# Kernel tuning notes

Hardware: AMD Instinct MI355X
Metric: run time of the kernel (lower is better)

The kernel has to match this reference:

```python
import jax, jax.numpy as jnp
import numpy as np

EPS_LN = 1e-6
EPS_NORM = 1e-12
MAX_SCALE_MUL = float(np.log(100.0))
H = 16  # num_heads


def _ln(x):
    # affine-free LayerNorm over last dim (torch uses biased variance)
    mu = jnp.mean(x, axis=-1, keepdims=True)
    var = jnp.mean((x - mu) ** 2, axis=-1, keepdims=True)
    return (x - mu) / jnp.sqrt(var + EPS_LN)


def _l2norm(x):
    n = jnp.sqrt(jnp.sum(x * x, axis=-1, keepdims=True))
    return x / jnp.maximum(n, EPS_NORM)


def setup_inputs() -> dict:
    key = jax.random.key(0)
    ks = jax.random.split(key, 12)
    B, L, C = 4, 1024, 1024
    Ccond, Dff = 1024, 4096
    s = lambda fan: 1.0 / np.sqrt(fan)
    return {
        "x": jax.random.normal(ks[0], (B, L, C), jnp.float32),
        "cond": jax.random.normal(ks[1], (B, Ccond), jnp.float32),
        "mat_qkv_w": jax.random.normal(ks[2], (3 * C, C), jnp.float32) * s(C),
        "q_bias": jnp.zeros((C,), jnp.float32),
        "v_bias": jnp.zeros((C,), jnp.float32),
        "scale_mul": jnp.full((1, H, 1, 1), np.log(4.0), jnp.float32),
        "proj_w": jax.random.normal(ks[3], (C, C), jnp.float32) * s(C),
        "proj_b": jnp.zeros((C,), jnp.float32),
        "ada_w": jax.random.normal(ks[4], (6 * C, Ccond), jnp.float32) * s(Ccond),
        "ada_b": jnp.zeros((6 * C,), jnp.float32),
        "fc1_w": jax.random.normal(ks[5], (Dff, C), jnp.float32) * s(C),
        "fc1_b": jnp.zeros((Dff,), jnp.float32),
        "fc2_w": jax.random.normal(ks[6], (C, Dff), jnp.float32) * s(Dff),
        "fc2_b": jnp.zeros((C,), jnp.float32),
    }


def reference(x, cond, mat_qkv_w, q_bias, v_bias, scale_mul, proj_w, proj_b,
              ada_w, ada_b, fc1_w, fc1_b, fc2_w, fc2_b):
    B, L, C = x.shape
    hd = C // H

    # AdaLN modulation params: SiLU -> Linear -> [B,1,6,C]
    ada = jax.nn.silu(cond) @ ada_w.T + ada_b
    ada = ada.reshape(B, 1, 6, C)
    gamma1, gamma2, scale1, scale2, shift1, shift2 = [ada[:, :, i] for i in range(6)]

    # --- attention branch ---
    x1 = _ln(x) * (scale1 + 1.0) + shift1
    qkv_bias = jnp.concatenate([q_bias, jnp.zeros_like(q_bias), v_bias])
    qkv = (x1 @ mat_qkv_w.T + qkv_bias).reshape(B, L, 3, H, hd)
    q, k, v = [jnp.transpose(qkv[:, :, i], (0, 2, 1, 3)) for i in range(3)]  # [B,H,L,hd]

    sm = jnp.exp(jnp.minimum(scale_mul, MAX_SCALE_MUL))  # [1,H,1,1]
    q = _l2norm(q) * sm
    k = _l2norm(k)

    scores = jnp.einsum('bhqd,bhkd->bhqk', q, k)  # scale = 1.0 under l2 norm
    probs = jax.nn.softmax(scores, axis=-1)
    o = jnp.einsum('bhqk,bhkd->bhqd', probs, v)
    o = jnp.transpose(o, (0, 2, 1, 3)).reshape(B, L, C)
    attn_out = o @ proj_w.T + proj_b
    x = x + attn_out * gamma1

    # --- FFN branch ---
    x2 = _ln(x) * (scale2 + 1.0) + shift2
    h = jax.nn.gelu(x2 @ fc1_w.T + fc1_b, approximate=False)
    ffn_out = h @ fc2_w.T + fc2_b
    x = x + ffn_out * gamma2
    return x
```

## Files before the change

kernel.cpp:

```cpp
#include <hip/hip_runtime.h>

typedef __bf16 bf16x8_t __attribute__((ext_vector_type(8)));
typedef bf16x8_t bf16x8 __attribute__((may_alias));
typedef float f32x4 __attribute__((ext_vector_type(4)));
typedef unsigned short u16x4 __attribute__((ext_vector_type(4)));
typedef unsigned short u16x8 __attribute__((ext_vector_type(8)));

#define DEV __device__ __forceinline__

DEV float b2f(unsigned short u) {
  union { unsigned int i; float f; } x; x.i = ((unsigned int)u) << 16; return x.f;
}
DEV unsigned short f2b(float f) {
  union { float f; unsigned int i; } x; x.f = f;
  return (unsigned short)((x.i + 0x7fffu + ((x.i >> 16) & 1u)) >> 16);
}

#define AS1(p) ((__attribute__((address_space(1))) void*)(p))
#define AS3(p) ((__attribute__((address_space(3))) void*)(p))

__global__ __launch_bounds__(256) void k_ada(const float* __restrict__ cond,
                                             const float* __restrict__ w,
                                             const float* __restrict__ bias,
                                             float* __restrict__ out) {
  __shared__ float sc[4096];
  int tt = threadIdx.x;
#pragma unroll
  for (int i = 0; i < 16; ++i) {
    float v = cond[tt + i * 256];
    sc[tt + i * 256] = v / (1.f + __expf(-v));
  }
  __syncthreads();
  int j = blockIdx.x * 4 + (tt >> 6);
  int lane = tt & 63;
  const float* wr = w + (size_t)j * 1024;
  float s0 = 0.f, s1 = 0.f, s2 = 0.f, s3 = 0.f;
#pragma unroll
  for (int u = 0; u < 4; ++u) {
    int k = u * 256 + lane * 4;
    float4 a = *(const float4*)(wr + k);
    float4 c0 = *(const float4*)(sc + k);
    float4 c1 = *(const float4*)(sc + 1024 + k);
    float4 c2 = *(const float4*)(sc + 2048 + k);
    float4 c3 = *(const float4*)(sc + 3072 + k);
    s0 += a.x * c0.x + a.y * c0.y + a.z * c0.z + a.w * c0.w;
    s1 += a.x * c1.x + a.y * c1.y + a.z * c1.z + a.w * c1.w;
    s2 += a.x * c2.x + a.y * c2.y + a.z * c2.z + a.w * c2.w;
    s3 += a.x * c3.x + a.y * c3.y + a.z * c3.z + a.w * c3.w;
  }
#pragma unroll
  for (int o = 1; o < 64; o <<= 1) {
    s0 += __shfl_xor(s0, o); s1 += __shfl_xor(s1, o);
    s2 += __shfl_xor(s2, o); s3 += __shfl_xor(s3, o);
  }
  if (lane == 0) {
    float bb = bias[j];
    out[j] = s0 + bb;
    out[6144 + j] = s1 + bb;
    out[12288 + j] = s2 + bb;
    out[18432 + j] = s3 + bb;
  }
}

__global__ __launch_bounds__(256) void k_castall(const float* __restrict__ q,
                                                 const float* __restrict__ p,
                                                 const float* __restrict__ f1,
                                                 const float* __restrict__ f2,
                                                 unsigned short* __restrict__ wq,
                                                 unsigned short* __restrict__ wp,
                                                 unsigned short* __restrict__ wf1,
                                                 unsigned short* __restrict__ wf2) {
  int i = blockIdx.x * 256 + threadIdx.x;
  for (int v = i; v < 3145728; v += 524288) {
    const float* s; unsigned short* d; int off;
    if (v < 786432) { s = q; d = wq; off = v; }
    else if (v < 1048576) { s = p; d = wp; off = v - 786432; }
    else if (v < 2097152) { s = f1; d = wf1; off = v - 1048576; }
    else { s = f2; d = wf2; off = v - 2097152; }
    float4 x = ((const float4*)s)[off];
    u16x4 o;
    o[0] = f2b(x.x); o[1] = f2b(x.y); o[2] = f2b(x.z); o[3] = f2b(x.w);
    *(u16x4*)(d + (size_t)off * 4) = o;
  }
}

__global__ __launch_bounds__(256) void k_ln_mod(const float* __restrict__ src,
                                                const float* __restrict__ ada,
                                                unsigned short* __restrict__ dst,
                                                int sidx, int hidx) {
  int row = blockIdx.x;
  int b = row >> 10;
  int t = threadIdx.x, lane = t & 63, wv = t >> 6;
  float4 v = *(const float4*)(src + (size_t)row * 1024 + t * 4);
  float s = v.x + v.y + v.z + v.w;
  float s2 = v.x * v.x + v.y * v.y + v.z * v.z + v.w * v.w;
#pragma unroll
  for (int o = 1; o < 64; o <<= 1) { s += __shfl_xor(s, o); s2 += __shfl_xor(s2, o); }
  __shared__ float red[8];
  if (lane == 0) { red[wv] = s; red[4 + wv] = s2; }
  __syncthreads();
  float ts = red[0] + red[1] + red[2] + red[3];
  float ts2 = red[4] + red[5] + red[6] + red[7];
  float mu = ts * (1.f / 1024.f);
  float var = ts2 * (1.f / 1024.f) - mu * mu;
  float rstd = rsqrtf(var + 1e-6f);
  const float* ar = ada + (size_t)b * 6144;
  float4 sc = *(const float4*)(ar + sidx * 1024 + t * 4);
  float4 sh = *(const float4*)(ar + hidx * 1024 + t * 4);
  u16x4 o;
  o[0] = f2b((v.x - mu) * rstd * (sc.x + 1.f) + sh.x);
  o[1] = f2b((v.y - mu) * rstd * (sc.y + 1.f) + sh.y);
  o[2] = f2b((v.z - mu) * rstd * (sc.z + 1.f) + sh.z);
  o[3] = f2b((v.w - mu) * rstd * (sc.w + 1.f) + sh.w);
  *(u16x4*)(dst + (size_t)row * 1024 + t * 4) = o;
}

template <int EPI, int SPLIT>
__global__ __launch_bounds__(512, 1) void k_gemm256(const unsigned short* __restrict__ A,
                                                    const unsigned short* __restrict__ W,
                                                    int N, int lda, int ldb, int nt,
                                                    const float* __restrict__ bias,
                                                    const float* __restrict__ qb,
                                                    const float* __restrict__ vb,
                                                    unsigned short* __restrict__ o0,
                                                    unsigned short* __restrict__ o1,
                                                    unsigned short* __restrict__ o2,
                                                    unsigned short* __restrict__ o3) {
  __shared__ unsigned short LDS[65536];
  const int tid = threadIdx.x;
  const int wv = tid >> 6, lane = tid & 63;
  const int fr = lane & 15, fg = lane >> 4;
  const int wm = wv >> 2, wn = wv & 3;

  const int cpx = gridDim.x >> 3;
  int wid = ((int)blockIdx.x & 7) * cpx + ((int)blockIdx.x >> 3);
  int sp = 0;
  if (SPLIT > 1) { sp = wid & (SPLIT - 1); wid >>= 2; }
  const int nx = N >> 8;
  const int m0 = (wid / nx) * 256, n0 = (wid % nx) * 256;
  const int kbase = sp * (nt << 6);
  unsigned short* outp = (SPLIT > 1) ? (sp == 0 ? o0 : sp == 1 ? o1 : sp == 2 ? o2 : o3) : o0;

  const int sRow = lane >> 2;
  const int sCh = (lane & 3) ^ ((lane >> 3) & 3);
  const unsigned short* aG = A + (size_t)(m0 + wv * 16 + sRow) * lda + kbase + sCh * 8;
  const unsigned short* bG = W + (size_t)(n0 + wv * 16 + sRow) * ldb + kbase + sCh * 8;

#define STQ4(qi_)                                                                              \
  {                                                                                            \
    const int wr_ = ((qi_)&3) * 16384;                                                         \
    const int ko_ = (qi_)*32;                                                                  \
    __builtin_amdgcn_global_load_lds(AS1(aG + ko_), AS3(LDS + wr_ + wv * 512), 16, 0, 0);      \
    __builtin_amdgcn_global_load_lds(AS1(aG + (size_t)128 * lda + ko_),                        \
                                     AS3(LDS + wr_ + 4096 + wv * 512), 16, 0, 0);              \
    __builtin_amdgcn_global_load_lds(AS1(bG + ko_), AS3(LDS + wr_ + 8192 + wv * 512), 16, 0, 0);\
    __builtin_amdgcn_global_load_lds(AS1(bG + (size_t)128 * ldb + ko_),                        \
                                     AS3(LDS + wr_ + 12288 + wv * 512), 16, 0, 0);             \
  }

  const int rswz = (fr >> 1) & 3;
  const int aOff = (wm * 128 + fr) * 32 + ((fg ^ rswz) << 3);
  const int bOff = 8192 + (wn * 64 + fr) * 32 + ((fg ^ rswz) << 3);

  f32x4 zz = {0.f, 0.f, 0.f, 0.f};
  f32x4 acc[8][4];
#pragma unroll
  for (int i = 0; i < 8; ++i)
#pragma unroll
    for (int j = 0; j < 4; ++j) acc[i][j] = zz;

  STQ4(0); STQ4(1); STQ4(2); STQ4(3);
  asm volatile("s_waitcnt vmcnt(8)" ::: "memory");
  __builtin_amdgcn_s_barrier();

#define LDSV(off) (*(const bf16x8*)(LDS + (off)))

  const int nIv = nt;
  for (int iv = 0; iv < nIv; ++iv) {
    if (iv >= 1) {
      const int t2 = 2 * iv + 2;
      if (t2 < 2 * nt) { STQ4(t2); STQ4(t2 + 1); }
    }
#pragma unroll
    for (int half = 0; half < 2; ++half) {
      const int rb = ((2 * iv + half) & 3) * 16384;
      bf16x8 bf0 = LDSV(rb + bOff);
      bf16x8 bf1 = LDSV(rb + bOff + 512);
      bf16x8 bf2 = LDSV(rb + bOff + 1024);
      bf16x8 bf3 = LDSV(rb + bOff + 1536);
      bf16x8 af[8];
#pragma unroll
      for (int mi = 0; mi < 8; ++mi) af[mi] = LDSV(rb + aOff + mi * 512);
#pragma unroll
      for (int mi = 0; mi < 8; ++mi) {
        acc[mi][0] = __builtin_amdgcn_mfma_f32_16x16x32_bf16(af[mi], bf0, acc[mi][0], 0, 0, 0);
        acc[mi][1] = __builtin_amdgcn_mfma_f32_16x16x32_bf16(af[mi], bf1, acc[mi][1], 0, 0, 0);
        acc[mi][2] = __builtin_amdgcn_mfma_f32_16x16x32_bf16(af[mi], bf2, acc[mi][2], 0, 0, 0);
        acc[mi][3] = __builtin_amdgcn_mfma_f32_16x16x32_bf16(af[mi], bf3, acc[mi][3], 0, 0, 0);
      }
    }
    if (iv < nIv - 1) {
      asm volatile("s_waitcnt vmcnt(0)" ::: "memory");
      __builtin_amdgcn_s_barrier();
    }
  }

#pragma unroll
  for (int mi = 0; mi < 8; ++mi) {
#pragma unroll
    for (int ni = 0; ni < 4; ++ni) {
#pragma unroll
      for (int r = 0; r < 4; ++r) {
        int m = m0 + wm * 128 + mi * 16 + fg * 4 + r;
        int n = n0 + wn * 64 + ni * 16 + fr;
        float v = acc[mi][ni][r];
        if constexpr (EPI == 0) {
          float bb = (n < 1024) ? qb[n] : ((n < 2048) ? 0.f : vb[n - 2048]);
          outp[(size_t)m * N + n] = f2b(v + bb);
        } else if constexpr (EPI == 2) {
          float z = v + bias[n];
          float u = z * (0.7978845608f + 0.0356774081f * z * z);
          float e = __expf(2.f * u);
          float th = 1.f - 2.f / (e + 1.f);
          outp[(size_t)m * N + n] = f2b(0.5f * z * (1.f + th));
        } else {
          outp[(size_t)m * N + n] = f2b(v);
        }
      }
    }
  }
#undef STQ4
#undef LDSV
}

__global__ __launch_bounds__(256) void k_fc2red(const unsigned short* __restrict__ P0,
                                                const unsigned short* __restrict__ P1,
                                                const unsigned short* __restrict__ P2,
                                                const unsigned short* __restrict__ P3,
                                                const float* __restrict__ xmid,
                                                const float* __restrict__ bias,
                                                const float* __restrict__ ada,
                                                float* __restrict__ out) {
  size_t idx = ((size_t)blockIdx.x * 256 + threadIdx.x) * 8;
  int n = (int)(idx & 1023);
  int b = (int)(idx >> 20);
  u16x8 v0 = *(const u16x8*)(P0 + idx);
  u16x8 v1 = *(const u16x8*)(P1 + idx);
  u16x8 v2 = *(const u16x8*)(P2 + idx);
  u16x8 v3 = *(const u16x8*)(P3 + idx);
  const float* gp = ada + (size_t)b * 6144 + 1024 + n;
  const float* bp = bias + n;
  const float* xp = xmid + idx;
  float* op = out + idx;
#pragma unroll
  for (int i = 0; i < 8; ++i) {
    float sum = b2f(v0[i]) + b2f(v1[i]) + b2f(v2[i]) + b2f(v3[i]);
    op[i] = xp[i] + (sum + bp[i]) * gp[i];
  }
}

__global__ __launch_bounds__(512) void k_gemm8(const unsigned short* __restrict__ A,
                                               const unsigned short* __restrict__ W,
                                               int M, int N, int K, int Khalf,
                                               const float* __restrict__ bias,
                                               const float* __restrict__ resid,
                                               const float* __restrict__ ada,
                                               float* __restrict__ outp) {
  __shared__ unsigned short SM[49152];
  const int t = threadIdx.x, lane = t & 63, wv = t >> 6;
  const int grp = wv >> 2, w4 = wv & 3;
  const int wr = w4 >> 1, wc = w4 & 1;
  const int cpx = gridDim.x >> 3;
  const int orig = blockIdx.x;
  const int wid = (orig & 7) * cpx + (orig >> 3);
  const int nx = N >> 7;
  const int m0 = (wid / nx) * 128, n0 = (wid % nx) * 128;

  f32x4 zz = {0.f, 0.f, 0.f, 0.f};
  f32x4 acc[4][4];
#pragma unroll
  for (int i = 0; i < 4; ++i)
#pragma unroll
    for (int j = 0; j < 4; ++j) acc[i][j] = zz;

  const int srow = lane >> 2, scol = (lane & 3) * 8;
  const int kbase = grp * Khalf;
  const unsigned short* aSrc0 = A + (size_t)(m0 + w4 * 16 + srow) * K + kbase + scol;
  const unsigned short* aSrc1 = aSrc0 + (size_t)64 * K;
  const unsigned short* bSrc0 = W + (size_t)(n0 + w4 * 16 + srow) * K + kbase + scol;
  const unsigned short* bSrc1 = bSrc0 + (size_t)64 * K;
  unsigned short* grpA = SM + grp * 24576;

  const int fr = lane & 15, fk = (lane >> 4) * 8;

#define STG8(buf_, k0_)                                                                            \
  {                                                                                                \
    __builtin_amdgcn_global_load_lds(AS1(aSrc0 + (k0_)), AS3(grpA + (buf_)*8192 + w4 * 512), 16, 0, 0); \
    __builtin_amdgcn_global_load_lds(AS1(aSrc1 + (k0_)), AS3(grpA + (buf_)*8192 + 2048 + w4 * 512), 16, 0, 0); \
    __builtin_amdgcn_global_load_lds(AS1(bSrc0 + (k0_)), AS3(grpA + (buf_)*8192 + 4096 + w4 * 512), 16, 0, 0); \
    __builtin_amdgcn_global_load_lds(AS1(bSrc1 + (k0_)), AS3(grpA + (buf_)*8192 + 6144 + w4 * 512), 16, 0, 0); \
  }

  const int nsteps = Khalf >> 5;
  STG8(0, 0);
  STG8(1, 32);
  asm volatile("s_waitcnt vmcnt(4)" ::: "memory");
  __builtin_amdgcn_s_barrier();

  for (int i = 0; i < nsteps; ++i) {
    const int buf = i % 3;
    if (i + 2 < nsteps) STG8((i + 2) % 3, (i + 2) * 32);
    const unsigned short* aRd = grpA + buf * 8192 + (wr * 64 + fr) * 32 + fk;
    const unsigned short* bRd = grpA + buf * 8192 + 4096 + (wc * 64 + fr) * 32 + fk;
    bf16x8 af[4], bfv[4];
#pragma unroll
    for (int q = 0; q < 4; ++q) af[q] = *(const bf16x8*)(aRd + q * 512);
#pragma unroll
    for (int q = 0; q < 4; ++q) bfv[q] = *(const bf16x8*)(bRd + q * 512);
#pragma unroll
    for (int mi = 0; mi < 4; ++mi)
#pragma unroll
      for (int ni = 0; ni < 4; ++ni)
        acc[mi][ni] = __builtin_amdgcn_mfma_f32_16x16x32_bf16(af[mi], bfv[ni], acc[mi][ni], 0, 0, 0);
    if (i < nsteps - 1) {
      if (i + 2 < nsteps) {
        asm volatile("s_waitcnt vmcnt(4)" ::: "memory");
      } else {
        asm volatile("s_waitcnt vmcnt(0)" ::: "memory");
      }
      __builtin_amdgcn_s_barrier();
    }
  }
  __syncthreads();

  float* xch = (float*)SM;
#pragma unroll
  for (int c = 0; c < 16; ++c) {
    if (grp == 1)
      *(f32x4*)&xch[c * 1024 + (w4 * 64 + lane) * 4] = acc[c >> 2][c & 3];
  }
  __syncthreads();
  if (grp == 1) return;
#pragma unroll
  for (int c = 0; c < 16; ++c) {
    f32x4 p = *(const f32x4*)&xch[c * 1024 + (w4 * 64 + lane) * 4];
    acc[c >> 2][c & 3] += p;
  }

  const int fg = lane >> 4;
#pragma unroll
  for (int mi = 0; mi < 4; ++mi) {
#pragma unroll
    for (int ni = 0; ni < 4; ++ni) {
#pragma unroll
      for (int r = 0; r < 4; ++r) {
        int m = m0 + wr * 64 + mi * 16 + fg * 4 + r;
        int n = n0 + wc * 64 + ni * 16 + fr;
        float v = acc[mi][ni][r];
        float g = ada[(size_t)(m >> 10) * 6144 + n];
        outp[(size_t)m * N + n] = resid[(size_t)m * N + n] + (v + bias[n]) * g;
      }
    }
  }
#undef STG8
}

__global__ __launch_bounds__(256) void k_qknorm(const unsigned short* __restrict__ qkv,
                                                const float* __restrict__ smul,
                                                unsigned short* __restrict__ Qn,
                                                unsigned short* __restrict__ Kn) {
  int row = blockIdx.x;
  int b = row >> 10, l = row & 1023;
  int t = threadIdx.x;
  int h = t >> 4, sl = t & 15;
  const unsigned short* base = qkv + (size_t)row * 3072 + h * 64 + sl * 4;
  size_t off = ((size_t)(b * 16 + h) * 1024 + l) * 64 + sl * 4;
  {
    u16x4 qv = *(const u16x4*)base;
    float q0 = b2f(qv[0]), q1 = b2f(qv[1]), q2 = b2f(qv[2]), q3 = b2f(qv[3]);
    float ss = q0 * q0 + q1 * q1 + q2 * q2 + q3 * q3;
#pragma unroll
    for (int o = 1; o < 16; o <<= 1) ss += __shfl_xor(ss, o);
    float sm = __expf(fminf(smul[h], 4.6051701859880914f));
    float qs = sm / fmaxf(sqrtf(ss), 1e-12f);
    u16x4 o; o[0] = f2b(q0 * qs); o[1] = f2b(q1 * qs); o[2] = f2b(q2 * qs); o[3] = f2b(q3 * qs);
    *(u16x4*)(Qn + off) = o;
  }
  {
    u16x4 kv = *(const u16x4*)(base + 1024);
    float k0 = b2f(kv[0]), k1 = b2f(kv[1]), k2 = b2f(kv[2]), k3 = b2f(kv[3]);
    float ss = k0 * k0 + k1 * k1 + k2 * k2 + k3 * k3;
#pragma unroll
    for (int o = 1; o < 16; o <<= 1) ss += __shfl_xor(ss, o);
    float ks = 1.f / fmaxf(sqrtf(ss), 1e-12f);
    u16x4 o; o[0] = f2b(k0 * ks); o[1] = f2b(k1 * ks); o[2] = f2b(k2 * ks); o[3] = f2b(k3 * ks);
    *(u16x4*)(Kn + off) = o;
  }
}

__global__ __launch_bounds__(256) void k_vtrans(const unsigned short* __restrict__ qkv,
                                                unsigned short* __restrict__ Vt) {
  int bh = blockIdx.y, b = bh >> 4, h = bh & 15;
  int l0 = blockIdx.x * 64;
  __shared__ unsigned short tile[64][72];
  int t = threadIdx.x;
  int lr = t >> 2, dp = (t & 3) * 16;
  const unsigned short* src = qkv + (size_t)(b * 1024 + l0 + lr) * 3072 + 2048 + h * 64 + dp;
  *(u16x8*)&tile[lr][dp] = *(const u16x8*)src;
  *(u16x8*)&tile[lr][dp + 8] = *(const u16x8*)(src + 8);
  __syncthreads();
  int d = t >> 2, lp = (t & 3) * 16;
  unsigned short ov[16];
#pragma unroll
  for (int j = 0; j < 16; ++j) {
    int p = lp + j;
    int l = ((p >> 5) * 2 + ((p >> 2) & 1)) * 16 + ((p >> 3) & 3) * 4 + (p & 3);
    ov[j] = tile[l][d];
  }
  unsigned short* dst = Vt + ((size_t)bh * 64 + d) * 1024 + l0 + lp;
  *(u16x8*)dst = *(u16x8*)&ov[0];
  *(u16x8*)(dst + 8) = *(u16x8*)&ov[8];
}

__global__ __launch_bounds__(256) void k_attn(const unsigned short* __restrict__ Qn,
                                              const unsigned short* __restrict__ Kn,
                                              const unsigned short* __restrict__ Vt,
                                              const float* __restrict__ smul,
                                              unsigned short* __restrict__ O) {
  const int qt = blockIdx.x, bh = blockIdx.y;
  const int b = bh >> 4, h = bh & 15;
  const int t = threadIdx.x, lane = t & 63, wv = t >> 6;
  const int fr = lane & 15, fg = lane >> 4;
  __shared__ unsigned short Kb[2][4096];
  __shared__ unsigned short Vb[2][4096];

  const int q0 = qt * 128 + wv * 32;
  const unsigned short* qp = Qn + ((size_t)bh * 1024 + q0 + fr) * 64 + fg * 8;
  bf16x8 qf00 = *(const bf16x8*)qp;
  bf16x8 qf01 = *(const bf16x8*)(qp + 32);
  bf16x8 qf10 = *(const bf16x8*)(qp + 1024);
  bf16x8 qf11 = *(const bf16x8*)(qp + 1024 + 32);

  const float M = __expf(fminf(smul[h], 4.6051701859880914f));

  const int srow = lane >> 3, sc = lane & 7;
  const int xr = (sc ^ srow) * 8;
  const unsigned short* kp0 = Kn + (size_t)bh * 65536 + (size_t)(wv * 16 + srow) * 64 + xr;
  const unsigned short* kp1 = kp0 + 8 * 64;
  const unsigned short* vp0 = Vt + (size_t)bh * 65536 + (size_t)(wv * 16 + srow) * 1024 + xr;
  const unsigned short* vp1 = vp0 + 8 * 1024;

  f32x4 zz = {0.f, 0.f, 0.f, 0.f};
  f32x4 oa0[4], oa1[4];
#pragma unroll
  for (int i = 0; i < 4; ++i) { oa0[i] = zz; oa1[i] = zz; }
  float ls0 = 0.f, ls1 = 0.f;

  {
    unsigned short* kd = &Kb[0][wv * 1024];
    unsigned short* vd = &Vb[0][wv * 1024];
    __builtin_amdgcn_global_load_lds(AS1(kp0), AS3(kd), 16, 0, 0);
    __builtin_amdgcn_global_load_lds(AS1(kp1), AS3(kd + 512), 16, 0, 0);
    __builtin_amdgcn_global_load_lds(AS1(vp0), AS3(vd), 16, 0, 0);
    __builtin_amdgcn_global_load_lds(AS1(vp1), AS3(vd + 512), 16, 0, 0);
  }
  __syncthreads();

  int cur = 0;
  for (int kv = 0; kv < 1024; kv += 64) {
    const int nxt = cur ^ 1;
    if (kv + 64 < 1024) {
      const int ko = (kv + 64) * 64;
      const int vo = kv + 64;
      unsigned short* kd = &Kb[nxt][wv * 1024];
      unsigned short* vd = &Vb[nxt][wv * 1024];
      __builtin_amdgcn_global_load_lds(AS1(kp0 + ko), AS3(kd), 16, 0, 0);
      __builtin_amdgcn_global_load_lds(AS1(kp1 + ko), AS3(kd + 512), 16, 0, 0);
      __builtin_amdgcn_global_load_lds(AS1(vp0 + vo), AS3(vd), 16, 0, 0);
      __builtin_amdgcn_global_load_lds(AS1(vp1 + vo), AS3(vd + 512), 16, 0, 0);
    }

    f32x4 s0[4], s1[4];
#pragma unroll
    for (int ct = 0; ct < 4; ++ct) {
      const int row = ct * 16 + fr, r7 = row & 7;
      const unsigned short* kr = &Kb[cur][row * 64];
      bf16x8 kf0 = *(const bf16x8*)(kr + ((fg ^ r7) << 3));
      bf16x8 kf1 = *(const bf16x8*)(kr + (((4 + fg) ^ r7) << 3));
      f32x4 z0 = __builtin_amdgcn_mfma_f32_16x16x32_bf16(kf0, qf00, zz, 0, 0, 0);
      s0[ct] = __builtin_amdgcn_mfma_f32_16x16x32_bf16(kf1, qf01, z0, 0, 0, 0);
      f32x4 z1 = __builtin_amdgcn_mfma_f32_16x16x32_bf16(kf0, qf10, zz, 0, 0, 0);
      s1[ct] = __builtin_amdgcn_mfma_f32_16x16x32_bf16(kf1, qf11, z1, 0, 0, 0);
    }

    bf16x8 pa0[2], pa1[2];
#pragma unroll
    for (int kg = 0; kg < 2; ++kg) {
      bf16x8 a0, a1;
#pragma unroll
      for (int c2 = 0; c2 < 2; ++c2) {
#pragma unroll
        for (int r = 0; r < 4; ++r) {
          float e0 = __expf(s0[kg * 2 + c2][r] - M);
          float e1 = __expf(s1[kg * 2 + c2][r] - M);
          ls0 += e0; ls1 += e1;
          a0[c2 * 4 + r] = (__bf16)e0;
          a1[c2 * 4 + r] = (__bf16)e1;
        }
      }
      pa0[kg] = a0; pa1[kg] = a1;
    }

#pragma unroll
    for (int kg = 0; kg < 2; ++kg) {
#pragma unroll
      for (int dt = 0; dt < 4; ++dt) {
        const int row = dt * 16 + fr, r7 = row & 7;
        bf16x8 vf = *(const bf16x8*)(&Vb[cur][row * 64] + ((((kg << 2) + fg) ^ r7) << 3));
        oa0[dt] = __builtin_amdgcn_mfma_f32_16x16x32_bf16(pa0[kg], vf, oa0[dt], 0, 0, 0);
        oa1[dt] = __builtin_amdgcn_mfma_f32_16x16x32_bf16(pa1[kg], vf, oa1[dt], 0, 0, 0);
      }
    }
    __syncthreads();
    cur = nxt;
  }

  ls0 += __shfl_xor(ls0, 16); ls0 += __shfl_xor(ls0, 32);
  ls1 += __shfl_xor(ls1, 16); ls1 += __shfl_xor(ls1, 32);

#pragma unroll
  for (int r = 0; r < 4; ++r) {
    float i0 = 1.f / __shfl(ls0, fg * 4 + r);
    float i1 = 1.f / __shfl(ls1, fg * 4 + r);
    unsigned short* ob = O + ((size_t)(b * 1024 + q0 + fg * 4 + r)) * 1024 + h * 64 + fr;
#pragma unroll
    for (int dt = 0; dt < 4; ++dt) {
      ob[dt * 16] = f2b(oa0[dt][r] * i0);
      ob[(size_t)16 * 1024 + dt * 16] = f2b(oa1[dt][r] * i1);
    }
  }
}

extern "C" void kernel_launch(void* const* d_in, const int* in_sizes, int n_in,
                              void* d_out, int out_size, void* d_ws, size_t ws_size,
                              hipStream_t stream) {
  const float* x        = (const float*)d_in[0];
  const float* cond     = (const float*)d_in[1];
  const float* qkv_w    = (const float*)d_in[2];
  const float* q_bias   = (const float*)d_in[3];
  const float* v_bias   = (const float*)d_in[4];
  const float* scale_mul= (const float*)d_in[5];
  const float* proj_w   = (const float*)d_in[6];
  const float* proj_b   = (const float*)d_in[7];
  const float* ada_w    = (const float*)d_in[8];
  const float* ada_b    = (const float*)d_in[9];
  const float* fc1_w    = (const float*)d_in[10];
  const float* fc1_b    = (const float*)d_in[11];
  const float* fc2_w    = (const float*)d_in[12];
  const float* fc2_b    = (const float*)d_in[13];
  float* out = (float*)d_out;
  char* ws = (char*)d_ws;

  unsigned short* WQ   = (unsigned short*)(ws + 0);
  unsigned short* WP   = (unsigned short*)(ws + 6291456);
  unsigned short* WF1  = (unsigned short*)(ws + 8388608);
  unsigned short* WF2  = (unsigned short*)(ws + 16777216);
  float*          ADA  = (float*)(ws + 25182208);
  unsigned short* X1   = (unsigned short*)(ws + 25280512);
  unsigned short* QKVB = (unsigned short*)(ws + 33669120);
  unsigned short* QN   = (unsigned short*)(ws + 58834944);
  unsigned short* KN   = (unsigned short*)(ws + 67223552);
  unsigned short* VT   = (unsigned short*)(ws + 75612160);
  unsigned short* OB   = (unsigned short*)(ws + 84000768);
  float*          XMID = (float*)(ws + 33669120);
  unsigned short* HB   = (unsigned short*)(ws + 50446336);
  unsigned short* FP0  = (unsigned short*)(ws + 0);
  unsigned short* FP1  = (unsigned short*)(ws + 8388608);
  unsigned short* FP2  = (unsigned short*)(ws + 25280512);
  unsigned short* FP3  = (unsigned short*)(ws + 84000768);

  (void)in_sizes; (void)n_in; (void)out_size; (void)ws_size;

  k_ada<<<1536, 256, 0, stream>>>(cond, ada_w, ada_b, ADA);
  k_castall<<<2048, 256, 0, stream>>>(qkv_w, proj_w, fc1_w, fc2_w, WQ, WP, WF1, WF2);

  k_ln_mod<<<4096, 256, 0, stream>>>(x, ADA, X1, 2, 4);
  k_gemm256<0, 1><<<192, 512, 0, stream>>>(X1, WQ, 3072, 1024, 1024, 16,
                                           nullptr, q_bias, v_bias, QKVB, nullptr, nullptr, nullptr);
  k_qknorm<<<4096, 256, 0, stream>>>(QKVB, scale_mul, QN, KN);
  k_vtrans<<<dim3(16, 64), 256, 0, stream>>>(QKVB, VT);
  k_attn<<<dim3(8, 64), 256, 0, stream>>>(QN, KN, VT, scale_mul, OB);
  k_gemm8<<<256, 512, 0, stream>>>(OB, WP, 4096, 1024, 1024, 512,
                                   proj_b, x, ADA, XMID);
  k_ln_mod<<<4096, 256, 0, stream>>>(XMID, ADA, X1, 3, 5);
  k_gemm256<2, 1><<<256, 512, 0, stream>>>(X1, WF1, 4096, 1024, 1024, 16,
                                           fc1_b, nullptr, nullptr, HB, nullptr, nullptr, nullptr);
  k_gemm256<4, 4><<<256, 512, 0, stream>>>(HB, WF2, 1024, 4096, 4096, 16,
                                           nullptr, nullptr, nullptr, FP0, FP1, FP2, FP3);
  k_fc2red<<<2048, 256, 0, stream>>>(FP0, FP1, FP2, FP3, XMID, fc2_b, ADA, out);
}
```

Before: 229.4 us.

## Shrink GEMM tile to 256x128 with 3-stage buffer and fuse QK L2-norm epilogue

The shared GEMM kernel moves from a 256x256 tile with a 4-slot LDS ring to a 256x128 tile with a 3-slot ring. LDS use drops to about 72KB, so more blocks can be resident per CU and the grids double. The QKV GEMM epilogue now applies the Q/K L2 normalisation and the scale_mul factor directly and writes Q/K in head-major layout. This removes the separate qknorm kernel and the round trip of the full QKV buffer through memory. The cost is lower data reuse per tile, and the workspace buffers are reassigned to new offsets.

```diff
diff --git a/kernel.cpp b/kernel.cpp
--- a/kernel.cpp
+++ b/kernel.cpp
@@ -116,7 +116,7 @@
 }
 
 template <int EPI, int SPLIT>
-__global__ __launch_bounds__(512, 1) void k_gemm256(const unsigned short* __restrict__ A,
+__global__ __launch_bounds__(512, 4) void k_gemm256(const unsigned short* __restrict__ A,
                                                     const unsigned short* __restrict__ W,
                                                     int N, int lda, int ldb, int nt,
                                                     const float* __restrict__ bias,
@@ -126,110 +126,143 @@
                                                     unsigned short* __restrict__ o1,
                                                     unsigned short* __restrict__ o2,
                                                     unsigned short* __restrict__ o3) {
-  __shared__ unsigned short LDS[65536];
+  __shared__ unsigned short LDS[36864];
   const int tid = threadIdx.x;
   const int wv = tid >> 6, lane = tid & 63;
   const int fr = lane & 15, fg = lane >> 4;
-  const int wm = wv >> 2, wn = wv & 3;
+  const int wm = wv >> 1, wn = wv & 1;
 
   const int cpx = gridDim.x >> 3;
   int wid = ((int)blockIdx.x & 7) * cpx + ((int)blockIdx.x >> 3);
   int sp = 0;
   if (SPLIT > 1) { sp = wid & (SPLIT - 1); wid >>= 2; }
-  const int nx = N >> 8;
-  const int m0 = (wid / nx) * 256, n0 = (wid % nx) * 256;
-  const int kbase = sp * (nt << 6);
+  const int nx = N >> 7;
+  const int m0 = (wid / nx) * 256, n0 = (wid % nx) * 128;
+  const int kbase = sp * (nt << 5);
   unsigned short* outp = (SPLIT > 1) ? (sp == 0 ? o0 : sp == 1 ? o1 : sp == 2 ? o2 : o3) : o0;
 
-  const int sRow = lane >> 2;
-  const int sCh = (lane & 3) ^ ((lane >> 3) & 3);
-  const unsigned short* aG = A + (size_t)(m0 + wv * 16 + sRow) * lda + kbase + sCh * 8;
-  const unsigned short* bG = W + (size_t)(n0 + wv * 16 + sRow) * ldb + kbase + sCh * 8;
-
-#define STQ4(qi_)                                                                              \
-  {                                                                                            \
-    const int wr_ = ((qi_)&3) * 16384;                                                         \
-    const int ko_ = (qi_)*32;                                                                  \
-    __builtin_amdgcn_global_load_lds(AS1(aG + ko_), AS3(LDS + wr_ + wv * 512), 16, 0, 0);      \
-    __builtin_amdgcn_global_load_lds(AS1(aG + (size_t)128 * lda + ko_),                        \
-                                     AS3(LDS + wr_ + 4096 + wv * 512), 16, 0, 0);              \
-    __builtin_amdgcn_global_load_lds(AS1(bG + ko_), AS3(LDS + wr_ + 8192 + wv * 512), 16, 0, 0);\
-    __builtin_amdgcn_global_load_lds(AS1(bG + (size_t)128 * ldb + ko_),                        \
-                                     AS3(LDS + wr_ + 12288 + wv * 512), 16, 0, 0);             \
+  const int sRow = tid >> 2;
+  const int sCh = (tid & 3) ^ ((tid >> 3) & 3);
+  const unsigned short* aG = A + (size_t)(m0 + sRow) * lda + kbase + sCh * 8;
+  const unsigned short* bG = W + (size_t)(n0 + sRow) * ldb + kbase + sCh * 8;
+
+#define STQ3(qi_)                                                                            \
+  {                                                                                          \
+    unsigned short* d_ = LDS + ((qi_) % 3) * 12288 + tid * 8;                                \
+    const int ko_ = (qi_) * 32;                                                              \
+    __builtin_amdgcn_global_load_lds(AS1(aG + ko_), AS3(d_), 16, 0, 0);                      \
+    __builtin_amdgcn_global_load_lds(AS1(aG + (size_t)128 * lda + ko_), AS3(d_ + 4096), 16, 0, 0); \
+    __builtin_amdgcn_global_load_lds(AS1(bG + ko_), AS3(d_ + 8192), 16, 0, 0);               \
   }
 
   const int rswz = (fr >> 1) & 3;
-  const int aOff = (wm * 128 + fr) * 32 + ((fg ^ rswz) << 3);
-  const int bOff = 8192 + (wn * 64 + fr) * 32 + ((fg ^ rswz) << 3);
+  const int xc = (fg ^ rswz) << 3;
+  const int aOff = (wm * 64 + fr) * 32 + xc;
+  const int bOff = 8192 + (wn * 64 + fr) * 32 + xc;
 
   f32x4 zz = {0.f, 0.f, 0.f, 0.f};
-  f32x4 acc[8][4];
-#pragma unroll
-  for (int i = 0; i < 8; ++i)
+  f32x4 acc[4][4];
+#pragma unroll
+  for (int i = 0; i < 4; ++i)
 #pragma unroll
     for (int j = 0; j < 4; ++j) acc[i][j] = zz;
 
-  STQ4(0); STQ4(1); STQ4(2); STQ4(3);
-  asm volatile("s_waitcnt vmcnt(8)" ::: "memory");
+  STQ3(0); STQ3(1); STQ3(2);
+  asm volatile("s_waitcnt vmcnt(6)" ::: "memory");
   __builtin_amdgcn_s_barrier();
 
 #define LDSV(off) (*(const bf16x8*)(LDS + (off)))
 
-  const int nIv = nt;
-  for (int iv = 0; iv < nIv; ++iv) {
-    if (iv >= 1) {
-      const int t2 = 2 * iv + 2;
-      if (t2 < 2 * nt) { STQ4(t2); STQ4(t2 + 1); }
-    }
-#pragma unroll
-    for (int half = 0; half < 2; ++half) {
-      const int rb = ((2 * iv + half) & 3) * 16384;
-      bf16x8 bf0 = LDSV(rb + bOff);
-      bf16x8 bf1 = LDSV(rb + bOff + 512);
-      bf16x8 bf2 = LDSV(rb + bOff + 1024);
-      bf16x8 bf3 = LDSV(rb + bOff + 1536);
-      bf16x8 af[8];
-#pragma unroll
-      for (int mi = 0; mi < 8; ++mi) af[mi] = LDSV(rb + aOff + mi * 512);
-#pragma unroll
-      for (int mi = 0; mi < 8; ++mi) {
-        acc[mi][0] = __builtin_amdgcn_mfma_f32_16x16x32_bf16(af[mi], bf0, acc[mi][0], 0, 0, 0);
-        acc[mi][1] = __builtin_amdgcn_mfma_f32_16x16x32_bf16(af[mi], bf1, acc[mi][1], 0, 0, 0);
-        acc[mi][2] = __builtin_amdgcn_mfma_f32_16x16x32_bf16(af[mi], bf2, acc[mi][2], 0, 0, 0);
-        acc[mi][3] = __builtin_amdgcn_mfma_f32_16x16x32_bf16(af[mi], bf3, acc[mi][3], 0, 0, 0);
+  for (int t = 0; t < nt; ++t) {
+    if (t >= 1 && t + 2 < nt) STQ3(t + 2);
+    const int REG = (t % 3) * 12288;
+    bf16x8 b0 = LDSV(REG + bOff);
+    bf16x8 b1 = LDSV(REG + bOff + 512);
+    bf16x8 b2 = LDSV(REG + bOff + 1024);
+    bf16x8 b3 = LDSV(REG + bOff + 1536);
+#pragma unroll
+    for (int mi = 0; mi < 4; ++mi) {
+      bf16x8 a = LDSV(REG + aOff + mi * 512);
+      acc[mi][0] = __builtin_amdgcn_mfma_f32_16x16x32_bf16(a, b0, acc[mi][0], 0, 0, 0);
+      acc[mi][1] = __builtin_amdgcn_mfma_f32_16x16x32_bf16(a, b1, acc[mi][1], 0, 0, 0);
+      acc[mi][2] = __builtin_amdgcn_mfma_f32_16x16x32_bf16(a, b2, acc[mi][2], 0, 0, 0);
+      acc[mi][3] = __builtin_amdgcn_mfma_f32_16x16x32_bf16(a, b3, acc[mi][3], 0, 0, 0);
+    }
+    if (t < nt - 1) {
+      if (t + 2 < nt) {
+        asm volatile("s_waitcnt vmcnt(3)" ::: "memory");
+      } else {
+        asm volatile("s_waitcnt vmcnt(0)" ::: "memory");
       }
-    }
-    if (iv < nIv - 1) {
-      asm volatile("s_waitcnt vmcnt(0)" ::: "memory");
       __builtin_amdgcn_s_barrier();
     }
   }
 
-#pragma unroll
-  for (int mi = 0; mi < 8; ++mi) {
-#pragma unroll
-    for (int ni = 0; ni < 4; ++ni) {
-#pragma unroll
-      for (int r = 0; r < 4; ++r) {
-        int m = m0 + wm * 128 + mi * 16 + fg * 4 + r;
-        int n = n0 + wn * 64 + ni * 16 + fr;
-        float v = acc[mi][ni][r];
-        if constexpr (EPI == 0) {
-          float bb = (n < 1024) ? qb[n] : ((n < 2048) ? 0.f : vb[n - 2048]);
-          outp[(size_t)m * N + n] = f2b(v + bb);
-        } else if constexpr (EPI == 2) {
-          float z = v + bias[n];
-          float u = z * (0.7978845608f + 0.0356774081f * z * z);
-          float e = __expf(2.f * u);
-          float th = 1.f - 2.f / (e + 1.f);
-          outp[(size_t)m * N + n] = f2b(0.5f * z * (1.f + th));
-        } else {
-          outp[(size_t)m * N + n] = f2b(v);
+  if constexpr (EPI == 0) {
+    const int nb = n0 + wn * 64;
+    if (nb < 2048) {
+      const bool isq = nb < 1024;
+      const int h = (nb & 1023) >> 6;
+      const float sm = isq ? __expf(fminf(bias[h], 4.6051701859880914f)) : 1.f;
+      unsigned short* obase = isq ? o0 : o1;
+#pragma unroll
+      for (int mi = 0; mi < 4; ++mi) {
+#pragma unroll
+        for (int r = 0; r < 4; ++r) {
+          float v0 = acc[mi][0][r], v1 = acc[mi][1][r], v2 = acc[mi][2][r], v3 = acc[mi][3][r];
+          if (isq) {
+            v0 += qb[nb + fr]; v1 += qb[nb + 16 + fr];
+            v2 += qb[nb + 32 + fr]; v3 += qb[nb + 48 + fr];
+          }
+          float ss = v0 * v0 + v1 * v1 + v2 * v2 + v3 * v3;
+          ss += __shfl_xor(ss, 1); ss += __shfl_xor(ss, 2);
+          ss += __shfl_xor(ss, 4); ss += __shfl_xor(ss, 8);
+          float scl = sm / fmaxf(sqrtf(ss), 1e-12f);
+          int m = m0 + wm * 64 + mi * 16 + fg * 4 + r;
+          int b = m >> 10, l = m & 1023;
+          unsigned short* dst = obase + ((size_t)(b * 16 + h) * 1024 + l) * 64 + fr;
+          dst[0]  = f2b(v0 * scl);
+          dst[16] = f2b(v1 * scl);
+          dst[32] = f2b(v2 * scl);
+          dst[48] = f2b(v3 * scl);
         }
       }
-    }
-  }
-#undef STQ4
+    } else {
+#pragma unroll
+      for (int mi = 0; mi < 4; ++mi)
+#pragma unroll
+        for (int ni = 0; ni < 4; ++ni)
+#pragma unroll
+          for (int r = 0; r < 4; ++r) {
+            int m = m0 + wm * 64 + mi * 16 + fg * 4 + r;
+            int n = nb + ni * 16 + fr - 2048;
+            o2[(size_t)m * 1024 + n] = f2b(acc[mi][ni][r] + vb[n]);
+          }
+    }
+  } else {
+#pragma unroll
+    for (int mi = 0; mi < 4; ++mi) {
+#pragma unroll
+      for (int ni = 0; ni < 4; ++ni) {
+#pragma unroll
+        for (int r = 0; r < 4; ++r) {
+          int m = m0 + wm * 64 + mi * 16 + fg * 4 + r;
+          int n = n0 + wn * 64 + ni * 16 + fr;
+          float v = acc[mi][ni][r];
+          if constexpr (EPI == 2) {
+            float z = v + bias[n];
+            float u = z * (0.7978845608f + 0.0356774081f * z * z);
+            float e = __expf(2.f * u);
+            float th = 1.f - 2.f / (e + 1.f);
+            outp[(size_t)m * N + n] = f2b(0.5f * z * (1.f + th));
+          } else {
+            outp[(size_t)m * N + n] = f2b(v);
+          }
+        }
+      }
+    }
+  }
+#undef STQ3
 #undef LDSV
 }
 
@@ -365,47 +398,14 @@
 #undef STG8
 }
 
-__global__ __launch_bounds__(256) void k_qknorm(const unsigned short* __restrict__ qkv,
-                                                const float* __restrict__ smul,
-                                                unsigned short* __restrict__ Qn,
-                                                unsigned short* __restrict__ Kn) {
-  int row = blockIdx.x;
-  int b = row >> 10, l = row & 1023;
-  int t = threadIdx.x;
-  int h = t >> 4, sl = t & 15;
-  const unsigned short* base = qkv + (size_t)row * 3072 + h * 64 + sl * 4;
-  size_t off = ((size_t)(b * 16 + h) * 1024 + l) * 64 + sl * 4;
-  {
-    u16x4 qv = *(const u16x4*)base;
-    float q0 = b2f(qv[0]), q1 = b2f(qv[1]), q2 = b2f(qv[2]), q3 = b2f(qv[3]);
-    float ss = q0 * q0 + q1 * q1 + q2 * q2 + q3 * q3;
-#pragma unroll
-    for (int o = 1; o < 16; o <<= 1) ss += __shfl_xor(ss, o);
-    float sm = __expf(fminf(smul[h], 4.6051701859880914f));
-    float qs = sm / fmaxf(sqrtf(ss), 1e-12f);
-    u16x4 o; o[0] = f2b(q0 * qs); o[1] = f2b(q1 * qs); o[2] = f2b(q2 * qs); o[3] = f2b(q3 * qs);
-    *(u16x4*)(Qn + off) = o;
-  }
-  {
-    u16x4 kv = *(const u16x4*)(base + 1024);
-    float k0 = b2f(kv[0]), k1 = b2f(kv[1]), k2 = b2f(kv[2]), k3 = b2f(kv[3]);
-    float ss = k0 * k0 + k1 * k1 + k2 * k2 + k3 * k3;
-#pragma unroll
-    for (int o = 1; o < 16; o <<= 1) ss += __shfl_xor(ss, o);
-    float ks = 1.f / fmaxf(sqrtf(ss), 1e-12f);
-    u16x4 o; o[0] = f2b(k0 * ks); o[1] = f2b(k1 * ks); o[2] = f2b(k2 * ks); o[3] = f2b(k3 * ks);
-    *(u16x4*)(Kn + off) = o;
-  }
-}
-
-__global__ __launch_bounds__(256) void k_vtrans(const unsigned short* __restrict__ qkv,
+__global__ __launch_bounds__(256) void k_vtrans(const unsigned short* __restrict__ V,
                                                 unsigned short* __restrict__ Vt) {
   int bh = blockIdx.y, b = bh >> 4, h = bh & 15;
   int l0 = blockIdx.x * 64;
   __shared__ unsigned short tile[64][72];
   int t = threadIdx.x;
   int lr = t >> 2, dp = (t & 3) * 16;
-  const unsigned short* src = qkv + (size_t)(b * 1024 + l0 + lr) * 3072 + 2048 + h * 64 + dp;
+  const unsigned short* src = V + (size_t)(b * 1024 + l0 + lr) * 1024 + h * 64 + dp;
   *(u16x8*)&tile[lr][dp] = *(const u16x8*)src;
   *(u16x8*)&tile[lr][dp + 8] = *(const u16x8*)(src + 8);
   __syncthreads();
@@ -567,17 +567,17 @@
   unsigned short* WF2  = (unsigned short*)(ws + 16777216);
   float*          ADA  = (float*)(ws + 25182208);
   unsigned short* X1   = (unsigned short*)(ws + 25280512);
-  unsigned short* QKVB = (unsigned short*)(ws + 33669120);
+  unsigned short* VB   = (unsigned short*)(ws + 33669120);
+  float*          XMID = (float*)(ws + 42057728);
   unsigned short* QN   = (unsigned short*)(ws + 58834944);
   unsigned short* KN   = (unsigned short*)(ws + 67223552);
   unsigned short* VT   = (unsigned short*)(ws + 75612160);
   unsigned short* OB   = (unsigned short*)(ws + 84000768);
-  float*          XMID = (float*)(ws + 33669120);
-  unsigned short* HB   = (unsigned short*)(ws + 50446336);
+  unsigned short* HB   = (unsigned short*)(ws + 58834944);
   unsigned short* FP0  = (unsigned short*)(ws + 0);
   unsigned short* FP1  = (unsigned short*)(ws + 8388608);
   unsigned short* FP2  = (unsigned short*)(ws + 25280512);
-  unsigned short* FP3  = (unsigned short*)(ws + 84000768);
+  unsigned short* FP3  = (unsigned short*)(ws + 33669120);
 
   (void)in_sizes; (void)n_in; (void)out_size; (void)ws_size;
 
@@ -585,17 +585,16 @@
   k_castall<<<2048, 256, 0, stream>>>(qkv_w, proj_w, fc1_w, fc2_w, WQ, WP, WF1, WF2);
 
   k_ln_mod<<<4096, 256, 0, stream>>>(x, ADA, X1, 2, 4);
-  k_gemm256<0, 1><<<192, 512, 0, stream>>>(X1, WQ, 3072, 1024, 1024, 16,
-                                           nullptr, q_bias, v_bias, QKVB, nullptr, nullptr, nullptr);
-  k_qknorm<<<4096, 256, 0, stream>>>(QKVB, scale_mul, QN, KN);
-  k_vtrans<<<dim3(16, 64), 256, 0, stream>>>(QKVB, VT);
+  k_gemm256<0, 1><<<384, 512, 0, stream>>>(X1, WQ, 3072, 1024, 1024, 32,
+                                           scale_mul, q_bias, v_bias, QN, KN, VB, nullptr);
+  k_vtrans<<<dim3(16, 64), 256, 0, stream>>>(VB, VT);
   k_attn<<<dim3(8, 64), 256, 0, stream>>>(QN, KN, VT, scale_mul, OB);
   k_gemm8<<<256, 512, 0, stream>>>(OB, WP, 4096, 1024, 1024, 512,
                                    proj_b, x, ADA, XMID);
   k_ln_mod<<<4096, 256, 0, stream>>>(XMID, ADA, X1, 3, 5);
-  k_gemm256<2, 1><<<256, 512, 0, stream>>>(X1, WF1, 4096, 1024, 1024, 16,
+  k_gemm256<2, 1><<<512, 512, 0, stream>>>(X1, WF1, 4096, 1024, 1024, 32,
                                            fc1_b, nullptr, nullptr, HB, nullptr, nullptr, nullptr);
-  k_gemm256<4, 4><<<256, 512, 0, stream>>>(HB, WF2, 1024, 4096, 4096, 16,
+  k_gemm256<4, 4><<<512, 512, 0, stream>>>(HB, WF2, 1024, 4096, 4096, 32,
                                            nullptr, nullptr, nullptr, FP0, FP1, FP2, FP3);
   k_fc2red<<<2048, 256, 0, stream>>>(FP0, FP1, FP2, FP3, XMID, fc2_b, ADA, out);
 }
```

Result: faster. 212.1 us (-7.5%).
